# Optimization experiments

Hardware: AMD Instinct MI355X
Metric: run time of the kernel (lower is better)

## Reference

```python
import jax, jax.numpy as jnp
import numpy as np

B, S, E, H = 4, 1024, 1024, 16
D = E // H
LN_EPS = 1e-5
W_SCALE = 0.02  # keep pre-softmax scores positive and moderate


def _linear(x, W, b):
    return x @ W + b


def _layernorm(x, g, b):
    m = jnp.mean(x, axis=-1, keepdims=True)
    v = jnp.mean((x - m) ** 2, axis=-1, keepdims=True)
    return (x - m) * jax.lax.rsqrt(v + LN_EPS) * g + b


def setup_inputs() -> dict:
    key = jax.random.key(0)
    ks = jax.random.split(key, 24)
    u = lambda k, shape, s=1.0: jax.random.uniform(k, shape, dtype=jnp.float32) * s
    inp = {
        'value': u(ks[0], (B, S, E)),
        'key':   u(ks[1], (B, S, E)),
        'query': u(ks[2], (B, S, E)),
        'mask':  jnp.ones((B, 1, 1, S), dtype=jnp.int32),
        # attention projections (W stored as [in, out])
        'Wv': u(ks[3], (E, E), W_SCALE), 'bv': u(ks[4], (E,), W_SCALE),
        'Wk': u(ks[5], (E, E), W_SCALE), 'bk': u(ks[6], (E,), W_SCALE),
        'Wq': u(ks[7], (E, E), W_SCALE), 'bq': u(ks[8], (E,), W_SCALE),
        'Wo': u(ks[9], (E, E), W_SCALE), 'bo': u(ks[10], (E,), W_SCALE),
        # feed-forward
        'W1': u(ks[11], (E, 4 * E), W_SCALE), 'b1': u(ks[12], (4 * E,), W_SCALE),
        'W2': u(ks[13], (4 * E, E), W_SCALE), 'b2': u(ks[14], (E,), W_SCALE),
        # layer norms
        'g1': jnp.ones((E,), jnp.float32), 'be1': jnp.zeros((E,), jnp.float32),
        'g2': jnp.ones((E,), jnp.float32), 'be2': jnp.zeros((E,), jnp.float32),
    }
    return inp


def reference(value, key, query, mask, Wv, bv, Wk, bk, Wq, bq, Wo, bo,
              W1, b1, W2, b2, g1, be1, g2, be2):
    b, q_len, _ = query.shape
    v = _linear(value, Wv, bv).reshape(b, -1, H, D)   # [B,K,H,D]
    k = _linear(key, Wk, bk).reshape(b, -1, H, D)     # [B,K,H,D]
    q = _linear(query, Wq, bq).reshape(b, q_len, H, D)
    att = jnp.einsum('bqhd,bkhd->bhqk', q, k)         # raw scores
    att = jnp.where(mask == 0, -jnp.inf, att)
    att = jnp.power(att, -0.5)                        # custom score^{-1/2} transform
    att = jax.nn.softmax(att, axis=3)
    ctx = jnp.einsum('bhqk,bkhd->bqhd', att, v).reshape(b, q_len, E)
    attn_out = _linear(ctx, Wo, bo)
    x = _layernorm(attn_out + query, g1, be1)         # dropout = identity (eval)
    ff = _linear(jax.nn.relu(_linear(x, W1, b1)), W2, b2)
    return _layernorm(ff + x, g2, be2)
```

## Files before the change

kernel.cpp:

```cpp
#include <hip/hip_runtime.h>
#include <hip/hip_bf16.h>
#include <cstdint>

typedef __hip_bfloat16 bf16;
typedef float f32x4 __attribute__((ext_vector_type(4)));
typedef short bf16x8 __attribute__((ext_vector_type(8)));
typedef short bf16x4v __attribute__((ext_vector_type(4)));

#define S_LEN 1024
#define EDIM  1024

__device__ __forceinline__ float bfs2f(short s) {
  return __uint_as_float(((unsigned)(unsigned short)s) << 16);
}
__device__ __forceinline__ short f2bfs(float f) {
  union { __hip_bfloat16 h; short s; } u;
  u.h = __float2bfloat16(f);
  return u.s;
}
__device__ __forceinline__ void glds16(const void* g, void* l) {
  __builtin_amdgcn_global_load_lds(
      (const __attribute__((address_space(1))) void*)g,
      (__attribute__((address_space(3))) void*)l, 16, 0, 0);
}
__device__ __forceinline__ float score_xform(float s) {
  float r, e;
  asm("v_rsq_f32 %0, %1" : "=v"(r) : "v"(s));
  r *= 1.44269504088896f;
  asm("v_exp_f32 %0, %1" : "=v"(e) : "v"(r));
  return e;
}
__device__ __forceinline__ int xcd_swz(int bid, int nwg) {
  const int q = nwg >> 3, r = nwg & 7, xcd = bid & 7, j = bid >> 3;
  return (xcd < r ? xcd * (q + 1) : r * (q + 1) + (xcd - r) * q) + j;
}
#define BAR() do { __builtin_amdgcn_s_barrier(); asm volatile("" ::: "memory"); } while (0)
#define WAITV(n) asm volatile("s_waitcnt vmcnt(" #n ")" ::: "memory")

struct Cvt3 { const float* in[3]; bf16* out[3]; };
__global__ __launch_bounds__(256)
void k_cvt3(Cvt3 p, int n4) {
  const float4* in = (const float4*)p.in[blockIdx.y];
  bf16x4v* out = (bf16x4v*)p.out[blockIdx.y];
  for (int i = blockIdx.x * 256 + threadIdx.x; i < n4; i += gridDim.x * 256) {
    float4 v = in[i];
    bf16x4v o;
    o[0] = f2bfs(v.x); o[1] = f2bfs(v.y); o[2] = f2bfs(v.z); o[3] = f2bfs(v.w);
    out[i] = o;
  }
}

struct TAll { const float* in[6]; bf16* out[6]; };
__global__ void k_transpose_all(TAll p) {
  int t = blockIdx.x;
  int z, tr, tc, R, C;
  if (t < 4096)      { z = t >> 10; R = 1024; C = 1024; int i = t & 1023; tr = i >> 5; tc = i & 31; }
  else if (t < 8192) { z = 4; R = 1024; C = 4096; int i = t - 4096; tr = i >> 7; tc = i & 127; }
  else               { z = 5; R = 4096; C = 1024; int i = t - 8192; tr = i >> 5; tc = i & 31; }
  __shared__ bf16 tile[32][33];
  const float* in = p.in[z];
  bf16* out = p.out[z];
  const int c0 = tc * 32, r0 = tr * 32;
  const int x = threadIdx.x;
  for (int yy = threadIdx.y; yy < 32; yy += 8)
    tile[yy][x] = __float2bfloat16(in[(size_t)(r0 + yy) * C + c0 + x]);
  __syncthreads();
  for (int yy = threadIdx.y; yy < 32; yy += 8)
    out[(size_t)(c0 + yy) * R + r0 + x] = tile[x][yy];
}

__global__ void k_transpose_v(const bf16* __restrict__ v, bf16* __restrict__ vt) {
  __shared__ bf16 t[32][33];
  const int bh = blockIdx.z;
  const bf16* in = v + (size_t)(bh >> 4) * S_LEN * EDIM + (bh & 15) * 64;
  bf16* out = vt + (size_t)bh * 64 * S_LEN;
  const int d0 = blockIdx.x * 32, s0 = blockIdx.y * 32;
  const int x = threadIdx.x;
  for (int yy = threadIdx.y; yy < 32; yy += 8)
    t[yy][x] = in[(size_t)(s0 + yy) * EDIM + d0 + x];
  __syncthreads();
  for (int yy = threadIdx.y; yy < 32; yy += 8)
    out[(size_t)(d0 + yy) * S_LEN + s0 + x] = t[x][yy];
}

template <int RELU, int OUT_F32, int HAS_BIAS>
__device__ __forceinline__ void gemm8_body(
    const bf16* __restrict__ A, int lda, const bf16* __restrict__ Bt, int ldb,
    const float* __restrict__ bias, void* __restrict__ Cout, int ldc,
    int K, int koff, int bm, int bn, char* smem) {
  const int tid = threadIdx.x, lane = tid & 63, wid = tid >> 6;
  const int wm = wid >> 2;
  const int wn = wid & 3;
  const int fr = lane & 15, fg = lane >> 4;
  const int sw = (fr & 7) << 4;

  const int rr = lane >> 3;
  const int cc = ((lane & 7) ^ rr) << 3;

  #define STG(src, ld, dstoff)                                                  \
    {                                                                           \
      const bf16* _s = (src);                                                   \
      _Pragma("unroll")                                                         \
      for (int _j = 0; _j < 2; _j++) {                                          \
        const int _L = wid * 2 + _j;                                            \
        glds16(_s + (size_t)(_L * 8 + rr) * (ld) + cc, smem + (dstoff) + _L * 1024); \
      }                                                                         \
    }

  const bf16* Abase = A + (size_t)bm * lda + koff;
  const bf16* Bbase = Bt + (size_t)bn * ldb + koff;
  const int nt = K >> 6;

  STG(Abase, lda, 0);
  STG(Abase + (size_t)128 * lda, lda, 16384);
  STG(Bbase, ldb, 32768);
  STG(Bbase + (size_t)128 * ldb, ldb, 49152);
  if (nt > 1) {
    STG(Bbase + 64, ldb, 65536 + 32768);
    STG(Bbase + (size_t)128 * ldb + 64, ldb, 65536 + 49152);
  }
  WAITV(0);
  BAR();

  f32x4 acc[8][4] = {};
  bf16x8 af[4][2], b01[2][2], b23[2][2];

  const int aRd = wm * 16384 + fr * 128;
  const int bRd = 32768 + (wn >> 1) * 16384 + (wn & 1) * 8192 + fr * 128;
  const int c0s = (0 * 64 + fg * 16) ^ sw;
  const int c1s = (1 * 64 + fg * 16) ^ sw;

  for (int n = 0; n < nt; n++) {
    const int buf = (n & 1) << 16;
    const int nbuf = buf ^ 65536;
    const char* sb = smem + buf;
    const int kA = (n + 1) << 6;
    const int kB = (n + 2) << 6;

#pragma unroll
    for (int i = 0; i < 4; i++) {
      af[i][0] = *(const bf16x8*)(sb + aRd + i * 2048 + c0s);
      af[i][1] = *(const bf16x8*)(sb + aRd + i * 2048 + c1s);
    }
#pragma unroll
    for (int j = 0; j < 2; j++) {
      b01[j][0] = *(const bf16x8*)(sb + bRd + j * 2048 + c0s);
      b01[j][1] = *(const bf16x8*)(sb + bRd + j * 2048 + c1s);
    }
    if (n + 1 < nt) STG(Abase + kA, lda, nbuf);
    BAR();
    __builtin_amdgcn_s_setprio(1);
#pragma unroll
    for (int i = 0; i < 4; i++)
#pragma unroll
      for (int j = 0; j < 2; j++) {
        acc[i][j] = __builtin_amdgcn_mfma_f32_16x16x32_bf16(af[i][0], b01[j][0], acc[i][j], 0, 0, 0);
        acc[i][j] = __builtin_amdgcn_mfma_f32_16x16x32_bf16(af[i][1], b01[j][1], acc[i][j], 0, 0, 0);
      }
    __builtin_amdgcn_s_setprio(0);
    BAR();

#pragma unroll
    for (int j = 0; j < 2; j++) {
      b23[j][0] = *(const bf16x8*)(sb + bRd + (j + 2) * 2048 + c0s);
      b23[j][1] = *(const bf16x8*)(sb + bRd + (j + 2) * 2048 + c1s);
    }
    if (n + 1 < nt) STG(Abase + (size_t)128 * lda + kA, lda, nbuf + 16384);
    BAR();
    __builtin_amdgcn_s_setprio(1);
#pragma unroll
    for (int i = 0; i < 4; i++)
#pragma unroll
      for (int j = 0; j < 2; j++) {
        acc[i][j + 2] = __builtin_amdgcn_mfma_f32_16x16x32_bf16(af[i][0], b23[j][0], acc[i][j + 2], 0, 0, 0);
        acc[i][j + 2] = __builtin_amdgcn_mfma_f32_16x16x32_bf16(af[i][1], b23[j][1], acc[i][j + 2], 0, 0, 0);
      }
    __builtin_amdgcn_s_setprio(0);
    BAR();

#pragma unroll
    for (int i = 0; i < 4; i++) {
      af[i][0] = *(const bf16x8*)(sb + aRd + (i + 4) * 2048 + c0s);
      af[i][1] = *(const bf16x8*)(sb + aRd + (i + 4) * 2048 + c1s);
    }
    if (n + 2 < nt) STG(Bbase + kB, ldb, buf + 32768);
    BAR();
    __builtin_amdgcn_s_setprio(1);
#pragma unroll
    for (int i = 0; i < 4; i++)
#pragma unroll
      for (int j = 0; j < 2; j++) {
        acc[i + 4][j + 2] = __builtin_amdgcn_mfma_f32_16x16x32_bf16(af[i][0], b23[j][0], acc[i + 4][j + 2], 0, 0, 0);
        acc[i + 4][j + 2] = __builtin_amdgcn_mfma_f32_16x16x32_bf16(af[i][1], b23[j][1], acc[i + 4][j + 2], 0, 0, 0);
      }
    __builtin_amdgcn_s_setprio(0);
    BAR();

    if (n + 2 < nt) STG(Bbase + (size_t)128 * ldb + kB, ldb, buf + 49152);
    __builtin_amdgcn_s_setprio(1);
#pragma unroll
    for (int i = 0; i < 4; i++)
#pragma unroll
      for (int j = 0; j < 2; j++) {
        acc[i + 4][j] = __builtin_amdgcn_mfma_f32_16x16x32_bf16(af[i][0], b01[j][0], acc[i + 4][j], 0, 0, 0);
        acc[i + 4][j] = __builtin_amdgcn_mfma_f32_16x16x32_bf16(af[i][1], b01[j][1], acc[i + 4][j], 0, 0, 0);
      }
    __builtin_amdgcn_s_setprio(0);
    if (n + 2 < nt) { WAITV(4); } else { WAITV(0); }
    BAR();
  }
  #undef STG

  float bv4[4];
#pragma unroll
  for (int j = 0; j < 4; j++)
    bv4[j] = HAS_BIAS ? bias[bn + wn * 64 + j * 16 + fr] : 0.f;
#pragma unroll
  for (int i = 0; i < 8; i++) {
    const size_t rowb = (size_t)bm + wm * 128 + i * 16 + fg * 4;
#pragma unroll
    for (int r = 0; r < 4; r++) {
#pragma unroll
      for (int j = 0; j < 4; j++) {
        float v = acc[i][j][r] + bv4[j];
        if (RELU) v = fmaxf(v, 0.f);
        const size_t idx = (rowb + r) * (size_t)ldc + bn + wn * 64 + j * 16 + fr;
        if (OUT_F32) ((float*)Cout)[idx] = v;
        else ((bf16*)Cout)[idx] = __float2bfloat16(v);
      }
    }
  }
}

struct G8Args {
  const bf16* A; int lda; const bf16* Bt; int ldb; const float* bias;
  void* C[4]; int ldc; int koffz[4]; int Kzz[4];
};
template <int RELU, int OUT_F32, int HAS_BIAS>
__global__ __launch_bounds__(512, 2)
void k_gemm8(G8Args a) {
  __shared__ __align__(16) char smem[131072];
  const int nwg = gridDim.x * gridDim.y;
  const int bid = xcd_swz(blockIdx.y * gridDim.x + blockIdx.x, nwg);
  const int bx = bid % gridDim.x, by = bid / gridDim.x;
  const int z = blockIdx.z;
  gemm8_body<RELU, OUT_F32, HAS_BIAS>(
      a.A, a.lda, a.Bt, a.ldb, a.bias, a.C[z], a.ldc,
      a.Kzz[z], a.koffz[z], by * 256, bx * 256, smem);
}

struct QkvArgs { const bf16* A[3]; const bf16* B[3]; const float* bias[3]; bf16* C[3]; };
__global__ __launch_bounds__(512, 2)
void k_gemm8_qkv(QkvArgs p) {
  __shared__ __align__(16) char smem[131072];
  const int nwg = gridDim.x * gridDim.y;
  const int bid = xcd_swz(blockIdx.y * gridDim.x + blockIdx.x, nwg);
  const int bx = bid % (int)gridDim.x;
  int by = bid / (int)gridDim.x;
  const int grp = by >> 4;
  by &= 15;
  gemm8_body<0, 0, 1>(p.A[grp], 1024, p.B[grp], 1024, p.bias[grp],
                      (void*)p.C[grp], 1024, 1024, 0, by * 256, bx * 256, smem);
}

__global__ __launch_bounds__(256)
void k_attn(const bf16* __restrict__ q, const bf16* __restrict__ k,
            const bf16* __restrict__ vt, bf16* __restrict__ ctx) {
  const int bh = blockIdx.x;
  const int qt = blockIdx.y;
  const int b = bh >> 4, h = bh & 15;
  const int tid = threadIdx.x, lane = tid & 63, w = tid >> 6;
  const int fr = lane & 15, fg = lane >> 4;
  const bf16* Q  = q  + (size_t)b * S_LEN * EDIM + h * 64;
  const bf16* Kp = k  + (size_t)b * S_LEN * EDIM + h * 64;
  const bf16* V  = vt + (size_t)bh * 64 * S_LEN;

  __shared__ __align__(16) bf16 lK[2][64 * 64];
  __shared__ __align__(16) bf16 lV[2][64 * 64];
  __shared__ __align__(16) bf16 eL[4][32][72];

  const int srow = lane >> 3;
  const int scol = (((lane & 7) ^ srow) << 3);
  const int rsw  = (fr & 7) << 3;

  bf16x8 qf[2][2];
#pragma unroll
  for (int i = 0; i < 2; i++)
#pragma unroll
    for (int ks = 0; ks < 2; ks++)
      qf[i][ks] = *(const bf16x8*)(Q + (size_t)(qt * 128 + w * 32 + i * 16 + fr) * EDIM + ks * 32 + fg * 8);

#pragma unroll
  for (int c = 0; c < 2; c++) {
    const int r = w * 8 + c * 32 + srow;
    glds16(Kp + (size_t)r * EDIM + scol, (char*)&lK[0][(w * 8 + c * 32) * 64]);
    glds16(V + (size_t)r * S_LEN + scol, (char*)&lV[0][(w * 8 + c * 32) * 64]);
  }
  __syncthreads();

  f32x4 accO[2][4] = {};
  float lsum[2][4] = {};
  int cur = 0;
  for (int kt = 0; kt < S_LEN; kt += 64) {
    if (kt + 64 < S_LEN) {
#pragma unroll
      for (int c = 0; c < 2; c++) {
        const int r = w * 8 + c * 32 + srow;
        glds16(Kp + (size_t)(kt + 64 + r) * EDIM + scol,
               (char*)&lK[cur ^ 1][(w * 8 + c * 32) * 64]);
        glds16(V + (size_t)r * S_LEN + kt + 64 + scol,
               (char*)&lV[cur ^ 1][(w * 8 + c * 32) * 64]);
      }
    }
    f32x4 accS[2][4] = {};
#pragma unroll
    for (int ks = 0; ks < 2; ks++)
#pragma unroll
      for (int j = 0; j < 4; j++) {
        bf16x8 kf = *(const bf16x8*)(&lK[cur][(j * 16 + fr) * 64 + ((ks * 32 + fg * 8) ^ rsw)]);
#pragma unroll
        for (int i = 0; i < 2; i++)
          accS[i][j] = __builtin_amdgcn_mfma_f32_16x16x32_bf16(qf[i][ks], kf, accS[i][j], 0, 0, 0);
      }
#pragma unroll
    for (int i = 0; i < 2; i++)
#pragma unroll
      for (int j = 0; j < 4; j++)
#pragma unroll
        for (int r = 0; r < 4; r++) {
          float p = score_xform(accS[i][j][r]);
          lsum[i][r] += p;
          eL[w][i * 16 + fg * 4 + r][j * 16 + fr] = __float2bfloat16(p);
        }
#pragma unroll
    for (int ks = 0; ks < 2; ks++) {
      bf16x8 af[2];
#pragma unroll
      for (int i = 0; i < 2; i++)
        af[i] = *(const bf16x8*)(&eL[w][i * 16 + fr][ks * 32 + fg * 8]);
#pragma unroll
      for (int j = 0; j < 4; j++) {
        bf16x8 vf = *(const bf16x8*)(&lV[cur][(j * 16 + fr) * 64 + ((ks * 32 + fg * 8) ^ rsw)]);
#pragma unroll
        for (int i = 0; i < 2; i++)
          accO[i][j] = __builtin_amdgcn_mfma_f32_16x16x32_bf16(af[i], vf, accO[i][j], 0, 0, 0);
      }
    }
    __syncthreads();
    cur ^= 1;
  }

#pragma unroll
  for (int i = 0; i < 2; i++)
#pragma unroll
    for (int r = 0; r < 4; r++) {
      float s = lsum[i][r];
      s += __shfl_xor(s, 1, 64);
      s += __shfl_xor(s, 2, 64);
      s += __shfl_xor(s, 4, 64);
      s += __shfl_xor(s, 8, 64);
      lsum[i][r] = s;
    }
#pragma unroll
  for (int i = 0; i < 2; i++)
#pragma unroll
    for (int r = 0; r < 4; r++) {
      const size_t qrow = (size_t)qt * 128 + w * 32 + i * 16 + fg * 4 + r;
      const float inv = 1.0f / lsum[i][r];
#pragma unroll
      for (int j = 0; j < 4; j++)
        ctx[((size_t)b * S_LEN + qrow) * EDIM + h * 64 + j * 16 + fr] =
            __float2bfloat16(accO[i][j][r] * inv);
    }
}

struct LnP { const float* p[4]; };
template <int NP, int RES_F32, int OUT_F32>
__global__ __launch_bounds__(256)
void k_ln_resN(LnP pp, const float* __restrict__ bias, const void* res_,
               const float* __restrict__ g, const float* __restrict__ be,
               void* out_) {
  const int row = blockIdx.x;
  const int tid = threadIdx.x;
  const int lane = tid & 63, wid = tid >> 6;
  const size_t base = (size_t)row * EDIM + tid * 4;
  float4 c = *(const float4*)(bias + tid * 4);
  float x[4] = {c.x, c.y, c.z, c.w};
#pragma unroll
  for (int t = 0; t < NP; t++) {
    float4 v = *(const float4*)(pp.p[t] + base);
    x[0] += v.x; x[1] += v.y; x[2] += v.z; x[3] += v.w;
  }
  if (RES_F32) {
    float4 v = *(const float4*)((const float*)res_ + base);
    x[0] += v.x; x[1] += v.y; x[2] += v.z; x[3] += v.w;
  } else {
    bf16x4v v = *(const bf16x4v*)((const bf16*)res_ + base);
#pragma unroll
    for (int i = 0; i < 4; i++) x[i] += bfs2f(v[i]);
  }

  float s = x[0] + x[1] + x[2] + x[3];
#pragma unroll
  for (int o = 32; o >= 1; o >>= 1) s += __shfl_xor(s, o, 64);
  __shared__ float red[4], red2[4];
  if (lane == 0) red[wid] = s;
  __syncthreads();
  const float mean = (red[0] + red[1] + red[2] + red[3]) * (1.0f / 1024.0f);

  float d[4], s2 = 0.f;
#pragma unroll
  for (int i = 0; i < 4; i++) { d[i] = x[i] - mean; s2 += d[i] * d[i]; }
#pragma unroll
  for (int o = 32; o >= 1; o >>= 1) s2 += __shfl_xor(s2, o, 64);
  if (lane == 0) red2[wid] = s2;
  __syncthreads();
  const float var = (red2[0] + red2[1] + red2[2] + red2[3]) * (1.0f / 1024.0f);
  const float inv = rsqrtf(var + 1e-5f);

  float4 g4 = *(const float4*)(g + tid * 4);
  float4 b4 = *(const float4*)(be + tid * 4);
  float o0 = d[0] * inv * g4.x + b4.x;
  float o1 = d[1] * inv * g4.y + b4.y;
  float o2 = d[2] * inv * g4.z + b4.z;
  float o3 = d[3] * inv * g4.w + b4.w;
  if (OUT_F32) {
    *(float4*)((float*)out_ + base) = make_float4(o0, o1, o2, o3);
  } else {
    bf16x4v o;
    o[0] = f2bfs(o0); o[1] = f2bfs(o1); o[2] = f2bfs(o2); o[3] = f2bfs(o3);
    *(bf16x4v*)((bf16*)out_ + base) = o;
  }
}

extern "C" void kernel_launch(void* const* d_in, const int* in_sizes, int n_in,
                              void* d_out, int out_size, void* d_ws, size_t ws_size,
                              hipStream_t stream) {
  const float* value = (const float*)d_in[0];
  const float* key_  = (const float*)d_in[1];
  const float* query = (const float*)d_in[2];
  const float* Wv = (const float*)d_in[4];  const float* bv = (const float*)d_in[5];
  const float* Wk = (const float*)d_in[6];  const float* bk = (const float*)d_in[7];
  const float* Wq = (const float*)d_in[8];  const float* bq = (const float*)d_in[9];
  const float* Wo = (const float*)d_in[10]; const float* bo = (const float*)d_in[11];
  const float* W1 = (const float*)d_in[12]; const float* b1 = (const float*)d_in[13];
  const float* W2 = (const float*)d_in[14]; const float* b2 = (const float*)d_in[15];
  const float* g1 = (const float*)d_in[16]; const float* be1 = (const float*)d_in[17];
  const float* g2 = (const float*)d_in[18]; const float* be2 = (const float*)d_in[19];

  char* wsb = (char*)d_ws;
  const size_t MB = 1024 * 1024;
  bf16* W1T = (bf16*)(wsb + 0 * MB);
  bf16* W2T = (bf16*)(wsb + 8 * MB);
  bf16* WqT = (bf16*)(wsb + 16 * MB);
  bf16* WkT = (bf16*)(wsb + 18 * MB);
  bf16* WvT = (bf16*)(wsb + 20 * MB);
  bf16* WoT = (bf16*)(wsb + 22 * MB);
  bf16* qx  = (bf16*)(wsb + 24 * MB);
  bf16* kx  = (bf16*)(wsb + 32 * MB);
  bf16* vx  = (bf16*)(wsb + 40 * MB);
  bf16* qb  = (bf16*)(wsb + 48 * MB);
  bf16* kb  = (bf16*)(wsb + 56 * MB);
  bf16* vb  = (bf16*)(wsb + 64 * MB);
  bf16* vtb = (bf16*)(wsb + 72 * MB);
  bf16* ctx = (bf16*)(wsb + 24 * MB);
  float* p0w = (float*)(wsb + 32 * MB);
  float* p1w = (float*)(wsb + 48 * MB);
  float* p2w = (float*)(wsb + 64 * MB);
  bf16* xb  = (bf16*)(wsb + 16 * MB);
  bf16* h1  = (bf16*)(wsb + 24 * MB);
  float* f1 = (float*)(wsb + 56 * MB);
  float* f2 = (float*)(wsb + 72 * MB);
  float* f3 = (float*)(wsb + 88 * MB);
  const int splitF = (ws_size >= 104 * MB) ? 4 : (ws_size >= 88 * MB) ? 3 : 2;

  const dim3 tb(32, 8);
  Cvt3 cp;
  cp.in[0] = query; cp.out[0] = qx;
  cp.in[1] = key_;  cp.out[1] = kx;
  cp.in[2] = value; cp.out[2] = vx;
  k_cvt3<<<dim3(1024, 3), 256, 0, stream>>>(cp, 1024 * 1024);

  TAll ta;
  ta.in[0] = Wq; ta.out[0] = WqT;
  ta.in[1] = Wk; ta.out[1] = WkT;
  ta.in[2] = Wv; ta.out[2] = WvT;
  ta.in[3] = Wo; ta.out[3] = WoT;
  ta.in[4] = W1; ta.out[4] = W1T;
  ta.in[5] = W2; ta.out[5] = W2T;
  k_transpose_all<<<12288, tb, 0, stream>>>(ta);

  QkvArgs qp;
  qp.A[0] = qx; qp.B[0] = WqT; qp.bias[0] = bq; qp.C[0] = qb;
  qp.A[1] = kx; qp.B[1] = WkT; qp.bias[1] = bk; qp.C[1] = kb;
  qp.A[2] = vx; qp.B[2] = WvT; qp.bias[2] = bv; qp.C[2] = vb;
  k_gemm8_qkv<<<dim3(4, 48), 512, 0, stream>>>(qp);

  k_transpose_v<<<dim3(2, 32, 64), tb, 0, stream>>>(vb, vtb);
  k_attn<<<dim3(64, 8), 256, 0, stream>>>(qb, kb, vtb, ctx);

  G8Args wo;
  wo.A = ctx; wo.lda = 1024; wo.Bt = WoT; wo.ldb = 1024; wo.bias = nullptr;
  wo.C[0] = p0w; wo.C[1] = p1w; wo.C[2] = p2w; wo.C[3] = nullptr;
  wo.ldc = 1024;
  wo.koffz[0] = 0;   wo.Kzz[0] = 384;
  wo.koffz[1] = 384; wo.Kzz[1] = 320;
  wo.koffz[2] = 704; wo.Kzz[2] = 320;
  wo.koffz[3] = 0;   wo.Kzz[3] = 64;
  k_gemm8<0, 1, 0><<<dim3(4, 16, 3), 512, 0, stream>>>(wo);
  LnP l1; l1.p[0] = p0w; l1.p[1] = p1w; l1.p[2] = p2w; l1.p[3] = nullptr;
  k_ln_resN<3, 1, 0><<<4096, 256, 0, stream>>>(l1, bo, query, g1, be1, xb);

  G8Args ff1;
  ff1.A = xb; ff1.lda = 1024; ff1.Bt = W1T; ff1.ldb = 1024; ff1.bias = b1;
  ff1.C[0] = h1; ff1.C[1] = nullptr; ff1.C[2] = nullptr; ff1.C[3] = nullptr;
  ff1.ldc = 4096;
  ff1.koffz[0] = 0; ff1.Kzz[0] = 1024;
  ff1.koffz[1] = 0; ff1.Kzz[1] = 64;
  ff1.koffz[2] = 0; ff1.Kzz[2] = 64;
  ff1.koffz[3] = 0; ff1.Kzz[3] = 64;
  k_gemm8<1, 0, 1><<<dim3(16, 16, 1), 512, 0, stream>>>(ff1);

  G8Args ff2;
  ff2.A = h1; ff2.lda = 4096; ff2.Bt = W2T; ff2.ldb = 4096; ff2.bias = nullptr;
  ff2.C[0] = d_out; ff2.C[1] = f1; ff2.C[2] = f2; ff2.C[3] = f3;
  ff2.ldc = 1024;
  if (splitF == 4) {
    for (int z = 0; z < 4; z++) { ff2.koffz[z] = z * 1024; ff2.Kzz[z] = 1024; }
  } else if (splitF == 3) {
    ff2.koffz[0] = 0;    ff2.Kzz[0] = 1344;
    ff2.koffz[1] = 1344; ff2.Kzz[1] = 1344;
    ff2.koffz[2] = 2688; ff2.Kzz[2] = 1408;
    ff2.koffz[3] = 0;    ff2.Kzz[3] = 64;
  } else {
    ff2.koffz[0] = 0;    ff2.Kzz[0] = 2048;
    ff2.koffz[1] = 2048; ff2.Kzz[1] = 2048;
    ff2.koffz[2] = 0;    ff2.Kzz[2] = 64;
    ff2.koffz[3] = 0;    ff2.Kzz[3] = 64;
  }
  k_gemm8<0, 1, 0><<<dim3(4, 16, splitF), 512, 0, stream>>>(ff2);

  LnP l2;
  l2.p[0] = (const float*)d_out; l2.p[1] = f1; l2.p[2] = f2; l2.p[3] = f3;
  if (splitF == 4)
    k_ln_resN<4, 0, 1><<<4096, 256, 0, stream>>>(l2, b2, xb, g2, be2, (float*)d_out);
  else if (splitF == 3)
    k_ln_resN<3, 0, 1><<<4096, 256, 0, stream>>>(l2, b2, xb, g2, be2, (float*)d_out);
  else
    k_ln_resN<2, 0, 1><<<4096, 256, 0, stream>>>(l2, b2, xb, g2, be2, (float*)d_out);
}
```

Measured before the change: 223.5 us.

## Load full A/B fragments upfront and cut GEMM main-loop barriers from four to two

The GEMM main loop now reads all A (8) and B (4) LDS fragments at the start of each k-step. It then runs two MFMA phases, so each iteration needs two barriers instead of four interleaved load/compute phases. The goal is less barrier stall and less LDS read interleaving. The cost is higher register use (24 bf16x8 fragments live), which may lower occupancy. The global-to-LDS prefetch issue points also change: both A halves are issued together, then both B halves.

```diff
diff --git a/kernel.cpp b/kernel.cpp
--- a/kernel.cpp
+++ b/kernel.cpp
@@ -123,7 +123,7 @@
   BAR();
 
   f32x4 acc[8][4] = {};
-  bf16x8 af[4][2], b01[2][2], b23[2][2];
+  bf16x8 af[8][2], bf[4][2];
 
   const int aRd = wm * 16384 + fr * 128;
   const int bRd = 32768 + (wn >> 1) * 16384 + (wn & 1) * 8192 + fr * 128;
@@ -138,72 +138,41 @@
     const int kB = (n + 2) << 6;
 
 #pragma unroll
-    for (int i = 0; i < 4; i++) {
+    for (int j = 0; j < 4; j++) {
+      bf[j][0] = *(const bf16x8*)(sb + bRd + j * 2048 + c0s);
+      bf[j][1] = *(const bf16x8*)(sb + bRd + j * 2048 + c1s);
+    }
+#pragma unroll
+    for (int i = 0; i < 8; i++) {
       af[i][0] = *(const bf16x8*)(sb + aRd + i * 2048 + c0s);
       af[i][1] = *(const bf16x8*)(sb + aRd + i * 2048 + c1s);
     }
-#pragma unroll
-    for (int j = 0; j < 2; j++) {
-      b01[j][0] = *(const bf16x8*)(sb + bRd + j * 2048 + c0s);
-      b01[j][1] = *(const bf16x8*)(sb + bRd + j * 2048 + c1s);
-    }
-    if (n + 1 < nt) STG(Abase + kA, lda, nbuf);
+    if (n + 1 < nt) {
+      STG(Abase + kA, lda, nbuf);
+      STG(Abase + (size_t)128 * lda + kA, lda, nbuf + 16384);
+    }
     BAR();
     __builtin_amdgcn_s_setprio(1);
 #pragma unroll
     for (int i = 0; i < 4; i++)
 #pragma unroll
-      for (int j = 0; j < 2; j++) {
-        acc[i][j] = __builtin_amdgcn_mfma_f32_16x16x32_bf16(af[i][0], b01[j][0], acc[i][j], 0, 0, 0);
-        acc[i][j] = __builtin_amdgcn_mfma_f32_16x16x32_bf16(af[i][1], b01[j][1], acc[i][j], 0, 0, 0);
+      for (int j = 0; j < 4; j++) {
+        acc[i][j] = __builtin_amdgcn_mfma_f32_16x16x32_bf16(af[i][0], bf[j][0], acc[i][j], 0, 0, 0);
+        acc[i][j] = __builtin_amdgcn_mfma_f32_16x16x32_bf16(af[i][1], bf[j][1], acc[i][j], 0, 0, 0);
       }
     __builtin_amdgcn_s_setprio(0);
-    BAR();
-
-#pragma unroll
-    for (int j = 0; j < 2; j++) {
-      b23[j][0] = *(const bf16x8*)(sb + bRd + (j + 2) * 2048 + c0s);
-      b23[j][1] = *(const bf16x8*)(sb + bRd + (j + 2) * 2048 + c1s);
-    }
-    if (n + 1 < nt) STG(Abase + (size_t)128 * lda + kA, lda, nbuf + 16384);
-    BAR();
+
+    if (n + 2 < nt) {
+      STG(Bbase + kB, ldb, buf + 32768);
+      STG(Bbase + (size_t)128 * ldb + kB, ldb, buf + 49152);
+    }
     __builtin_amdgcn_s_setprio(1);
 #pragma unroll
     for (int i = 0; i < 4; i++)
 #pragma unroll
-      for (int j = 0; j < 2; j++) {
-        acc[i][j + 2] = __builtin_amdgcn_mfma_f32_16x16x32_bf16(af[i][0], b23[j][0], acc[i][j + 2], 0, 0, 0);
-        acc[i][j + 2] = __builtin_amdgcn_mfma_f32_16x16x32_bf16(af[i][1], b23[j][1], acc[i][j + 2], 0, 0, 0);
-      }
-    __builtin_amdgcn_s_setprio(0);
-    BAR();
-
-#pragma unroll
-    for (int i = 0; i < 4; i++) {
-      af[i][0] = *(const bf16x8*)(sb + aRd + (i + 4) * 2048 + c0s);
-      af[i][1] = *(const bf16x8*)(sb + aRd + (i + 4) * 2048 + c1s);
-    }
-    if (n + 2 < nt) STG(Bbase + kB, ldb, buf + 32768);
-    BAR();
-    __builtin_amdgcn_s_setprio(1);
-#pragma unroll
-    for (int i = 0; i < 4; i++)
-#pragma unroll
-      for (int j = 0; j < 2; j++) {
-        acc[i + 4][j + 2] = __builtin_amdgcn_mfma_f32_16x16x32_bf16(af[i][0], b23[j][0], acc[i + 4][j + 2], 0, 0, 0);
-        acc[i + 4][j + 2] = __builtin_amdgcn_mfma_f32_16x16x32_bf16(af[i][1], b23[j][1], acc[i + 4][j + 2], 0, 0, 0);
-      }
-    __builtin_amdgcn_s_setprio(0);
-    BAR();
-
-    if (n + 2 < nt) STG(Bbase + (size_t)128 * ldb + kB, ldb, buf + 49152);
-    __builtin_amdgcn_s_setprio(1);
-#pragma unroll
-    for (int i = 0; i < 4; i++)
-#pragma unroll
-      for (int j = 0; j < 2; j++) {
-        acc[i + 4][j] = __builtin_amdgcn_mfma_f32_16x16x32_bf16(af[i][0], b01[j][0], acc[i + 4][j], 0, 0, 0);
-        acc[i + 4][j] = __builtin_amdgcn_mfma_f32_16x16x32_bf16(af[i][1], b01[j][1], acc[i + 4][j], 0, 0, 0);
+      for (int j = 0; j < 4; j++) {
+        acc[i + 4][j] = __builtin_amdgcn_mfma_f32_16x16x32_bf16(af[i + 4][0], bf[j][0], acc[i + 4][j], 0, 0, 0);
+        acc[i + 4][j] = __builtin_amdgcn_mfma_f32_16x16x32_bf16(af[i + 4][1], bf[j][1], acc[i + 4][j], 0, 0, 0);
       }
     __builtin_amdgcn_s_setprio(0);
     if (n + 2 < nt) { WAITV(4); } else { WAITV(0); }
```

Result: no change. 223.6 us (+0.0%).
